# Kernel tuning notes

Measured on AMD Instinct MI355X. Metric: run time of the kernel, lower is better.

The kernel has to match this reference:

```python
import jax, jax.numpy as jnp
import numpy as np

B, S, H, P2 = 64, 512, 768, 46  # batch, seq, hidden, num_p*2


def setup_inputs() -> dict:
    key = jax.random.key(0)
    k1, k2, k3, k4 = jax.random.split(key, 4)
    hidden_states = jax.random.normal(k1, (B, S, H), dtype=jnp.float32)
    # subject start/end indices must lie within the valid (masked-in) prefix
    lengths = jax.random.randint(k2, (B,), S // 4, S + 1)  # cue lengths per sample
    input_mask = (jnp.arange(S)[None, :] < lengths[:, None]).astype(jnp.int32)
    ids = jax.random.randint(k3, (B, 2), 0, S // 4)
    batch_subject_ids = jnp.sort(ids, axis=1).astype(jnp.int32)
    W = jax.random.normal(k4, (P2, H), dtype=jnp.float32) * (1.0 / np.sqrt(H))
    b = jnp.zeros((P2,), dtype=jnp.float32)
    return {"hidden_states": hidden_states, "batch_subject_ids": batch_subject_ids,
            "input_mask": input_mask, "W": W, "b": b}


def reference(hidden_states, batch_subject_ids, input_mask, W, b):
    # per-sample subject embedding: h[b, start] + h[b, end]  -> [B, H]
    batch_idx = jnp.arange(hidden_states.shape[0])
    s = (hidden_states[batch_idx, batch_subject_ids[:, 0]]
         + hidden_states[batch_idx, batch_subject_ids[:, 1]])
    # broadcast-add s to the first cue_len positions of each sample
    cue_len = jnp.sum(input_mask, axis=1)  # [B]
    pos_mask = (jnp.arange(hidden_states.shape[1])[None, :] < cue_len[:, None])  # [B, S]
    h = hidden_states + s[:, None, :] * pos_mask[:, :, None].astype(hidden_states.dtype)
    # linear + sigmoid^4 (dropout is identity in eval mode)
    logits = jnp.einsum('bsh,ph->bsp', h, W) + b
    return jax.nn.sigmoid(logits) ** 4
```

## Files before the change

### kernel.cpp

```cpp
#include <hip/hip_runtime.h>
#include <hip/hip_bf16.h>

#define SEQ 512
#define HID 768
#define P2  46
#define MT  16
#define BLK 256
#define NSTEP (HID / 32)
#define QSTRIDE 48

typedef short bf16x8 __attribute__((ext_vector_type(8)));
typedef float f32x4  __attribute__((ext_vector_type(4)));

__device__ __forceinline__ unsigned short f2bf(float f) {
  union { float f; unsigned int u; } v; v.f = f;
  return (unsigned short)((v.u + 0x7FFFu + ((v.u >> 16) & 1u)) >> 16);
}

__device__ __forceinline__ unsigned short fcvt(float f) {
  __hip_bfloat16 x = __float2bfloat16(f);
  return *reinterpret_cast<unsigned short*>(&x);
}

__device__ __forceinline__ void async_ld16(const void* g, void* l) {
  __builtin_amdgcn_global_load_lds(
      (const __attribute__((address_space(1))) unsigned int*)g,
      (__attribute__((address_space(3))) unsigned int*)l, 16, 0, 0);
}

__global__ __launch_bounds__(64) void prep_kernel(
    const float* __restrict__ h, const int* __restrict__ ids,
    const float* __restrict__ W, unsigned short* __restrict__ Wb,
    float* __restrict__ q) {
  int b = blockIdx.x, p = blockIdx.y, lane = threadIdx.x;
  const float* w = W + (size_t)p * HID;
  if (b == 0) {
    #pragma unroll
    for (int j = 0; j < HID / 64; ++j)
      Wb[p * HID + lane + j * 64] = f2bf(w[lane + j * 64]);
    if (p < 2) {
      #pragma unroll
      for (int j = 0; j < HID / 64; ++j)
        Wb[(P2 + p) * HID + lane + j * 64] = 0;
    }
  }
  int i0 = ids[b * 2 + 0], i1 = ids[b * 2 + 1];
  const float* r0 = h + ((size_t)b * SEQ + i0) * HID;
  const float* r1 = h + ((size_t)b * SEQ + i1) * HID;
  float acc = 0.f;
  #pragma unroll
  for (int j = 0; j < HID / 64; ++j) {
    int k = lane + j * 64;
    acc += (r0[k] + r1[k]) * w[k];
  }
  #pragma unroll
  for (int off = 32; off > 0; off >>= 1) acc += __shfl_down(acc, off, 64);
  if (lane == 0) q[b * QSTRIDE + p] = acc;
}

__global__ __launch_bounds__(BLK, 3) void main_kernel(
    const float* __restrict__ h, const int* __restrict__ mask,
    const unsigned short* __restrict__ Wb, const float* __restrict__ bias,
    const float* __restrict__ q, float* __restrict__ out) {
  __shared__ __align__(16) float hA[MT][HID];

  const int tid  = threadIdx.x;
  const int lane = tid & 63, wv = tid >> 6;
  const int mr = lane & 15, qd = lane >> 4;
  const int row0 = blockIdx.x * MT;
  const int b    = row0 >> 9;

  const float* hblk = h + (size_t)row0 * HID;
  #pragma unroll
  for (int j = 0; j < 12; ++j) {
    const int r   = (wv << 2) + j / 3;
    const int seg = j % 3;
    int c  = (seg << 6) + lane;
    int gg = c >> 1;
    int gs = (gg & ~7) | ((gg ^ r) & 7);
    const float* src = hblk + (size_t)r * HID + ((gs << 1) | (c & 1)) * 4;
    async_ld16(src, &hA[r][seg << 8]);
  }

  const int nt = wv;
  bf16x8 wf[NSTEP];
  f32x4 acc = f32x4{0.f, 0.f, 0.f, 0.f};
  int mk = 0, p0 = 0, grow = 0;
  float bv[4], qv[4];
  if (wv < 3) {
    const unsigned short* wbp = Wb + (size_t)((nt << 4) + mr) * HID + (qd << 3);
    #pragma unroll
    for (int s = 0; s < NSTEP; ++s)
      wf[s] = *(const bf16x8*)(wbp + (s << 5));
    grow = row0 + mr;
    mk   = mask[grow];
    p0   = (nt << 4) + (qd << 2);
    const float* qrow = q + b * QSTRIDE;
    #pragma unroll
    for (int i = 0; i < 4; ++i) {
      bv[i] = (p0 + i < P2) ? bias[p0 + i] : 0.f;
      qv[i] = qrow[p0 + i];
    }
  }

  __syncthreads();
  if (wv >= 3) return;

  #pragma unroll
  for (int s = 0; s < NSTEP; ++s) {
    int gg = (s << 2) + qd;
    int gs = (gg & ~7) | ((gg ^ mr) & 7);
    const float* fp = &hA[mr][gs << 3];
    float4 a0 = *(const float4*)fp;
    float4 a1 = *(const float4*)(fp + 4);
    bf16x8 hb = { (short)fcvt(a0.x), (short)fcvt(a0.y),
                  (short)fcvt(a0.z), (short)fcvt(a0.w),
                  (short)fcvt(a1.x), (short)fcvt(a1.y),
                  (short)fcvt(a1.z), (short)fcvt(a1.w) };
    acc = __builtin_amdgcn_mfma_f32_16x16x32_bf16(wf[s], hb, acc, 0, 0, 0);
  }

  float* orow = out + (size_t)grow * P2;
  float o[4];
  #pragma unroll
  for (int i = 0; i < 4; ++i) {
    float x = acc[i] + bv[i] + (mk ? qv[i] : 0.f);
    float sg = 1.f / (1.f + __expf(-x));
    sg *= sg; sg *= sg;
    o[i] = sg;
  }
  if (p0 + 1 < P2) *(float2*)(orow + p0)     = make_float2(o[0], o[1]);
  if (p0 + 3 < P2) *(float2*)(orow + p0 + 2) = make_float2(o[2], o[3]);
}

extern "C" void kernel_launch(void* const* d_in, const int* in_sizes, int n_in,
                              void* d_out, int out_size, void* d_ws, size_t ws_size,
                              hipStream_t stream) {
  const float* h    = (const float*)d_in[0];
  const int*   ids  = (const int*)d_in[1];
  const int*   mask = (const int*)d_in[2];
  const float* W    = (const float*)d_in[3];
  const float* bias = (const float*)d_in[4];
  float* out = (float*)d_out;

  unsigned short* Wb = (unsigned short*)d_ws;
  float* q = (float*)((char*)d_ws + 48 * HID * sizeof(unsigned short));

  prep_kernel<<<dim3(64, P2), 64, 0, stream>>>(h, ids, W, Wb, q);
  main_kernel<<<dim3((64 * SEQ) / MT), BLK, 0, stream>>>(h, mask, Wb, bias, q, out);
}
```

Before: 164.5 us.

## Fuse weight conversion and subject projection into main GEMM kernel

Removes the separate prep kernel. Each main block now loads fp32 W directly and converts it to bf16 in registers. Each wave also recomputes the per-sample subject projection q from the two subject rows and gathers it with shuffles. This drops one kernel launch and the workspace round trip. In exchange, every block (2048 of them) redundantly reads W plus two hidden rows and does extra FMAs. Padded rows 46–47 now use clamped W rows instead of zeros, and their outputs are discarded.

Result: slower. 317.2 us (+92.8%).

```diff
diff --git a/kernel.cpp b/kernel.cpp
--- a/kernel.cpp
+++ b/kernel.cpp
@@ -7,15 +7,9 @@
 #define MT  16
 #define BLK 256
 #define NSTEP (HID / 32)
-#define QSTRIDE 48
 
 typedef short bf16x8 __attribute__((ext_vector_type(8)));
 typedef float f32x4  __attribute__((ext_vector_type(4)));
-
-__device__ __forceinline__ unsigned short f2bf(float f) {
-  union { float f; unsigned int u; } v; v.f = f;
-  return (unsigned short)((v.u + 0x7FFFu + ((v.u >> 16) & 1u)) >> 16);
-}
 
 __device__ __forceinline__ unsigned short fcvt(float f) {
   __hip_bfloat16 x = __float2bfloat16(f);
@@ -28,40 +22,10 @@
       (__attribute__((address_space(3))) unsigned int*)l, 16, 0, 0);
 }
 
-__global__ __launch_bounds__(64) void prep_kernel(
+__global__ __launch_bounds__(BLK, 3) void fused_kernel(
     const float* __restrict__ h, const int* __restrict__ ids,
-    const float* __restrict__ W, unsigned short* __restrict__ Wb,
-    float* __restrict__ q) {
-  int b = blockIdx.x, p = blockIdx.y, lane = threadIdx.x;
-  const float* w = W + (size_t)p * HID;
-  if (b == 0) {
-    #pragma unroll
-    for (int j = 0; j < HID / 64; ++j)
-      Wb[p * HID + lane + j * 64] = f2bf(w[lane + j * 64]);
-    if (p < 2) {
-      #pragma unroll
-      for (int j = 0; j < HID / 64; ++j)
-        Wb[(P2 + p) * HID + lane + j * 64] = 0;
-    }
-  }
-  int i0 = ids[b * 2 + 0], i1 = ids[b * 2 + 1];
-  const float* r0 = h + ((size_t)b * SEQ + i0) * HID;
-  const float* r1 = h + ((size_t)b * SEQ + i1) * HID;
-  float acc = 0.f;
-  #pragma unroll
-  for (int j = 0; j < HID / 64; ++j) {
-    int k = lane + j * 64;
-    acc += (r0[k] + r1[k]) * w[k];
-  }
-  #pragma unroll
-  for (int off = 32; off > 0; off >>= 1) acc += __shfl_down(acc, off, 64);
-  if (lane == 0) q[b * QSTRIDE + p] = acc;
-}
-
-__global__ __launch_bounds__(BLK, 3) void main_kernel(
-    const float* __restrict__ h, const int* __restrict__ mask,
-    const unsigned short* __restrict__ Wb, const float* __restrict__ bias,
-    const float* __restrict__ q, float* __restrict__ out) {
+    const int* __restrict__ mask, const float* __restrict__ W,
+    const float* __restrict__ bias, float* __restrict__ out) {
   __shared__ __align__(16) float hA[MT][HID];
 
   const int tid  = threadIdx.x;
@@ -88,18 +52,42 @@
   int mk = 0, p0 = 0, grow = 0;
   float bv[4], qv[4];
   if (wv < 3) {
-    const unsigned short* wbp = Wb + (size_t)((nt << 4) + mr) * HID + (qd << 3);
+    const int p = (nt << 4) + mr;
+    const int wrow = (p > P2 - 1) ? (P2 - 1) : p;
+    const float* wp = W + (size_t)wrow * HID + (qd << 3);
+    const int i0 = ids[b * 2 + 0], i1 = ids[b * 2 + 1];
+    const float* h0p = h + ((size_t)b * SEQ + i0) * HID + (qd << 3);
+    const float* h1p = h + ((size_t)b * SEQ + i1) * HID + (qd << 3);
+
+    float qa = 0.f, qb = 0.f;
     #pragma unroll
-    for (int s = 0; s < NSTEP; ++s)
-      wf[s] = *(const bf16x8*)(wbp + (s << 5));
+    for (int s = 0; s < NSTEP; ++s) {
+      float4 w0 = *(const float4*)(wp  + (s << 5));
+      float4 w1 = *(const float4*)(wp  + (s << 5) + 4);
+      float4 a0 = *(const float4*)(h0p + (s << 5));
+      float4 a1 = *(const float4*)(h0p + (s << 5) + 4);
+      float4 b0 = *(const float4*)(h1p + (s << 5));
+      float4 b1 = *(const float4*)(h1p + (s << 5) + 4);
+      wf[s] = bf16x8{ (short)fcvt(w0.x), (short)fcvt(w0.y),
+                      (short)fcvt(w0.z), (short)fcvt(w0.w),
+                      (short)fcvt(w1.x), (short)fcvt(w1.y),
+                      (short)fcvt(w1.z), (short)fcvt(w1.w) };
+      qa += w0.x * (a0.x + b0.x);  qb += w0.y * (a0.y + b0.y);
+      qa += w0.z * (a0.z + b0.z);  qb += w0.w * (a0.w + b0.w);
+      qa += w1.x * (a1.x + b1.x);  qb += w1.y * (a1.y + b1.y);
+      qa += w1.z * (a1.z + b1.z);  qb += w1.w * (a1.w + b1.w);
+    }
+    float qfull = qa + qb;
+    qfull += __shfl_xor(qfull, 16, 64);
+    qfull += __shfl_xor(qfull, 32, 64);
+
     grow = row0 + mr;
     mk   = mask[grow];
     p0   = (nt << 4) + (qd << 2);
-    const float* qrow = q + b * QSTRIDE;
     #pragma unroll
     for (int i = 0; i < 4; ++i) {
       bv[i] = (p0 + i < P2) ? bias[p0 + i] : 0.f;
-      qv[i] = qrow[p0 + i];
+      qv[i] = __shfl(qfull, (qd << 2) + i, 64);
     }
   }
 
@@ -143,9 +131,5 @@
   const float* bias = (const float*)d_in[4];
   float* out = (float*)d_out;
 
-  unsigned short* Wb = (unsigned short*)d_ws;
-  float* q = (float*)((char*)d_ws + 48 * HID * sizeof(unsigned short));
-
-  prep_kernel<<<dim3(64, P2), 64, 0, stream>>>(h, ids, W, Wb, q);
-  main_kernel<<<dim3((64 * SEQ) / MT), BLK, 0, stream>>>(h, mask, Wb, bias, q, out);
+  fused_kernel<<<dim3((64 * SEQ) / MT), BLK, 0, stream>>>(h, ids, mask, W, bias, out);
 }
```
